# Kernel optimization log

Measured on AMD Instinct MI355X. Metric: run time of the kernel, lower is better.

Reference implementation:

```python
import jax, jax.numpy as jnp
import numpy as np

D_MODEL = 1024
N_HEADS = 16
D_HEAD = D_MODEL // N_HEADS


def setup_inputs() -> dict:
    key = jax.random.key(0)
    ks = jax.random.split(key, 9)
    s = 1.0 / np.sqrt(D_MODEL)
    def lin(kw, kb):
        W = jax.random.uniform(kw, (D_MODEL, D_MODEL), jnp.float32, -s, s)
        b = jax.random.uniform(kb, (D_MODEL,), jnp.float32, -s, s)
        return W, b
    Wq, bq = lin(ks[0], ks[1])
    Wk, bk = lin(ks[2], ks[3])
    Wv, bv = lin(ks[4], ks[5])
    Wo, bo = lin(ks[6], ks[7])
    x = jax.random.normal(ks[8], (4, 2048, D_MODEL), jnp.float32)
    return {"x": x, "Wq": Wq, "bq": bq, "Wk": Wk, "bk": bk,
            "Wv": Wv, "bv": bv, "Wo": Wo, "bo": bo}


def reference(x, Wq, bq, Wk, bk, Wv, bv, Wo, bo):
    B, T, C = x.shape
    # torch Linear: y = x @ W.T + b
    Q = x @ Wq.T + bq
    K = x @ Wk.T + bk
    V = x @ Wv.T + bv
    # [B, H, T, Dh]
    Q = Q.reshape(B, T, N_HEADS, D_HEAD).transpose(0, 2, 1, 3)
    K = K.reshape(B, T, N_HEADS, D_HEAD).transpose(0, 2, 1, 3)
    V = V.reshape(B, T, N_HEADS, D_HEAD).transpose(0, 2, 1, 3)
    scale = jnp.float32(np.sqrt(D_HEAD))
    scores = jnp.einsum('bhqd,bhkd->bhqk', Q, K) / scale
    causal = jnp.tril(jnp.ones((T, T), dtype=bool))  # True where allowed
    scores = jnp.where(causal, scores, jnp.float32(-jnp.inf))
    attn = jax.nn.softmax(scores, axis=-1)
    out = jnp.einsum('bhqk,bhkd->bhqd', attn, V)
    out = out.transpose(0, 2, 1, 3).reshape(B, T, C)
    return out @ Wo.T + bo
```

## Files before the change

### kernel.cpp

```cpp
#include <hip/hip_runtime.h>
#include <hip/hip_bf16.h>


typedef float f32x4 __attribute__((ext_vector_type(4)));
typedef __bf16 bf16x8 __attribute__((ext_vector_type(8)));

#define DEVI __device__ __forceinline__

#define QSCALE 0.1803368801111204f

template<int N> struct IC { static constexpr int value = N; };

DEVI ushort f2b(float x) {
  __hip_bfloat16 h = __float2bfloat16(x);
  return __builtin_bit_cast(ushort, h);
}

DEVI unsigned int pkbf(float a, float b) {
#if __has_builtin(__builtin_amdgcn_cvt_pk_bf16_f32)
  typedef __bf16 bf16x2 __attribute__((ext_vector_type(2)));
  bf16x2 r = __builtin_amdgcn_cvt_pk_bf16_f32(a, b);
  return __builtin_bit_cast(unsigned int, r);
#else
  return (unsigned int)f2b(a) | ((unsigned int)f2b(b) << 16);
#endif
}

DEVI bf16x8 ldsFrag(const ushort* p) {
  return __builtin_bit_cast(bf16x8, *(const uint4*)p);
}

DEVI f32x4 mfma16(bf16x8 a, bf16x8 b, f32x4 c) {
  return __builtin_amdgcn_mfma_f32_16x16x32_bf16(a, b, c, 0, 0, 0);
}

DEVI void gload_lds16(const ushort* g, ushort* l) {
  __builtin_amdgcn_global_load_lds(
      (const __attribute__((address_space(1))) unsigned int*)g,
      (__attribute__((address_space(3))) unsigned int*)l, 16, 0, 0);
}

#define SBAR() do { __builtin_amdgcn_sched_barrier(0); \
                    __builtin_amdgcn_s_barrier();      \
                    __builtin_amdgcn_sched_barrier(0); } while (0)

__global__ void k_cvtAll(const float4* __restrict__ x,
                         const float4* __restrict__ w0, const float4* __restrict__ w1,
                         const float4* __restrict__ w2, const float4* __restrict__ w3,
                         ushort4* __restrict__ xb, ushort4* __restrict__ wcat) {
  const int blk = blockIdx.x;
  const int i = blk * 256 + threadIdx.x;
  float4 f;
  ushort4* dst;
  int di;
  if (blk < 8192) {
    f = x[i]; dst = xb; di = i;
  } else {
    const int wi = i - 8192 * 256;
    const int sel = wi >> 18;
    const float4* src = (sel == 0) ? w0 : (sel == 1) ? w1 : (sel == 2) ? w2 : w3;
    f = src[wi & 262143]; dst = wcat; di = wi;
  }
  ushort4 o;
  o.x = f2b(f.x); o.y = f2b(f.y); o.z = f2b(f.z); o.w = f2b(f.w);
  dst[di] = o;
}

template<int MODE>
__global__ __launch_bounds__(512, 2)
void k_gemm(const ushort* __restrict__ A, const ushort* __restrict__ W,
            const float* __restrict__ b0, const float* __restrict__ b1,
            const float* __restrict__ b2, float* __restrict__ outF,
            ushort* __restrict__ oQ, ushort* __restrict__ oK, ushort* __restrict__ oV) {
  __shared__ ushort As[3 * 128 * 64];
  __shared__ ushort Bs[3 * 256 * 64];
  const int tid = threadIdx.x;
  const int wave = tid >> 6, lane = tid & 63;
  const int col = lane & 15, quad = lane >> 4;
  const int id = blockIdx.x;
  const int s_ = id >> 3;
  const int m0 = ((id & 7) * 8 + (s_ & 7)) * 128;
  const int n0 = (s_ >> 3) * 256;
  const int wm = (wave >> 2) * 64, wn = (wave & 3) * 64;
  f32x4 acc[4][4] = {};

  const int grow = lane >> 3;
  const int gchunk = ((lane & 7) ^ grow) * 8;
  const int cswz = col & 7;
  const ushort* Ag = A + (size_t)(m0 + wave * 16 + grow) * 1024 + gchunk;
  const ushort* Wg = W + (size_t)(n0 + wave * 32 + grow) * 1024 + gchunk;
  ushort* AsW = &As[wave * 1024];
  ushort* BsW = &Bs[wave * 2048];

  const int matId = (MODE == 0) ? (n0 >> 10) : 0;

  auto stageA = [&](int ks, int sb) {
    gload_lds16(Ag + ks,        AsW + sb * 8192);
    gload_lds16(Ag + ks + 8192, AsW + sb * 8192 + 512);
  };
  auto stageBh = [&](int ks, int sb, int h) {
    const ushort* sp = Wg + ks + h * 16384;
    ushort* dp = BsW + sb * 16384 + h * 1024;
    gload_lds16(sp,        dp);
    gload_lds16(sp + 8192, dp + 512);
  };

  auto kloop = [&](auto swc) {
    auto phase = [&](int cur, int kk, auto stagef) {
      const int ko = ((kk * 4 + quad) ^ cswz) * 8;
      const ushort* Ab = &As[cur * 8192];
      const ushort* Bb = &Bs[cur * 16384];
      bf16x8 af[4], bfr[4];
#pragma unroll
      for (int i = 0; i < 4; ++i)
        af[i] = ldsFrag(&Ab[(wm + i * 16 + col) * 64 + ko]);
#pragma unroll
      for (int j = 0; j < 4; ++j)
        bfr[j] = ldsFrag(&Bb[(wn + j * 16 + col) * 64 + ko]);
      stagef();
      SBAR();
      __builtin_amdgcn_s_setprio(1);
#pragma unroll
      for (int i = 0; i < 4; ++i)
#pragma unroll
        for (int j = 0; j < 4; ++j) {
          if constexpr (decltype(swc)::value != 0)
            acc[i][j] = mfma16(bfr[j], af[i], acc[i][j]);
          else
            acc[i][j] = mfma16(af[i], bfr[j], acc[i][j]);
        }
      __builtin_amdgcn_s_setprio(0);
    };

    stageA(0, 0);  stageBh(0, 0, 0);  stageBh(0, 0, 1);
    stageA(64, 1); stageBh(64, 1, 0); stageBh(64, 1, 1);
    asm volatile("s_waitcnt vmcnt(6)" ::: "memory");
    SBAR();

    int r0 = 0, r1 = 1, r2 = 2;
    for (int t = 0; t < 14; ++t) {
      const int ks = (t + 2) * 64;
      phase(r0, 0, [&] { stageA(ks, r2); stageBh(ks, r2, 0); });
      SBAR();
      phase(r0, 1, [&] { stageBh(ks, r2, 1); });
      asm volatile("s_waitcnt vmcnt(6)" ::: "memory");
      SBAR();
      const int tmp = r0; r0 = r1; r1 = r2; r2 = tmp;
    }
    phase(r0, 0, [&] {});
    SBAR();
    phase(r0, 1, [&] {});
    asm volatile("s_waitcnt vmcnt(0)" ::: "memory");
    SBAR();
    phase(r1, 0, [&] {});
    SBAR();
    phase(r1, 1, [&] {});
  };

  if (MODE == 1 || matId < 2) kloop(IC<1>{}); else kloop(IC<0>{});

  if (MODE == 1) {
#pragma unroll
    for (int j = 0; j < 4; ++j) {
      const int nb = n0 + wn + j * 16 + quad * 4;
      const float4 bb = *(const float4*)&b0[nb];
#pragma unroll
      for (int i = 0; i < 4; ++i) {
        const int m = m0 + wm + i * 16 + col;
        float4 v;
        v.x = acc[i][j][0] + bb.x;
        v.y = acc[i][j][1] + bb.y;
        v.z = acc[i][j][2] + bb.z;
        v.w = acc[i][j][3] + bb.w;
        *(float4*)&outF[(size_t)m * 1024 + nb] = v;
      }
    }
  } else if (matId < 2) {
    ushort* dst = (matId == 0) ? oQ : oK;
    const float* bias = (matId == 0) ? b0 : b1;
    const float sc = (matId == 0) ? QSCALE : 1.0f;
#pragma unroll
    for (int j = 0; j < 4; ++j) {
      const int nl = ((n0 & 1023) + wn + j * 16 + quad * 4);
      const int h = nl >> 6, dh0 = nl & 63;
      const float4 bb = *(const float4*)&bias[nl];
#pragma unroll
      for (int i = 0; i < 4; ++i) {
        const int m = m0 + wm + i * 16 + col;
        const int b = m >> 11, t = m & 2047;
        ushort4 pk;
        pk.x = f2b((acc[i][j][0] + bb.x) * sc);
        pk.y = f2b((acc[i][j][1] + bb.y) * sc);
        pk.z = f2b((acc[i][j][2] + bb.z) * sc);
        pk.w = f2b((acc[i][j][3] + bb.w) * sc);
        *(ushort4*)&dst[(((size_t)(b * 16 + h) * 2048) + t) * 64 + dh0] = pk;
      }
    }
  } else {
#pragma unroll
    for (int j = 0; j < 4; ++j) {
      const int nl = ((n0 & 1023) + wn + j * 16 + col);
      const int h = nl >> 6, dh = nl & 63;
      const float bn = b2[nl];
#pragma unroll
      for (int i = 0; i < 4; ++i) {
        const int mBase = m0 + wm + i * 16 + quad * 4;
        const int b = mBase >> 11, t = mBase & 2047;
        ushort4 pk;
        pk.x = f2b(acc[i][j][0] + bn);
        pk.y = f2b(acc[i][j][1] + bn);
        pk.z = f2b(acc[i][j][2] + bn);
        pk.w = f2b(acc[i][j][3] + bn);
        *(ushort4*)&oV[(((size_t)(b * 16 + h) * 64) + dh) * 2048 + t] = pk;
      }
    }
  }
}

__global__ __launch_bounds__(512, 4)
void k_attn(const ushort* __restrict__ Q, const ushort* __restrict__ K,
            const ushort* __restrict__ Vt, ushort* __restrict__ AO) {
  __shared__ ushort Ks[2 * 4096];
  __shared__ ushort Vs[2 * 4096];
  __shared__ ushort Os[512];
  __shared__ ushort Ps[16 * 16 * 72];
  const int tid = threadIdx.x;
  const int wave = tid >> 6, lane = tid & 63;
  const int col = lane & 15, quad = lane >> 4;
  const int id = blockIdx.x;
  const int bh = (id & 7) * 8 + ((id >> 3) & 7);
  const int g = id >> 6;
  const int t = (id < 256) ? (7 - g) : (g - 4);
  const int q0 = t * 256;
  const ushort* Qg = Q + (size_t)bh * 2048 * 64;
  const ushort* Kg = K + (size_t)bh * 2048 * 64;
  const ushort* Vg = Vt + (size_t)bh * 64 * 2048;

  if (tid < 128) {
    const ushort one = 0x3F80;
    ushort4 zv;
    if (tid < 8) { zv.x = one; zv.y = one; zv.z = one; zv.w = one; }
    else         { zv.x = 0;   zv.y = 0;   zv.z = 0;   zv.w = 0;   }
    *(ushort4*)&Os[tid * 4] = zv;
  }

  const int grow = lane >> 3;
  const int gchunk = ((lane & 7) ^ grow) * 8;
  const int cswz = col & 7;
  ushort* Pw0 = &Ps[((wave * 2 + 0) * 16 + col) * 72];
  ushort* Pw1 = &Ps[((wave * 2 + 1) * 16 + col) * 72];

  bf16x8 qf[2][2];
#pragma unroll
  for (int s = 0; s < 2; ++s) {
    const ushort* p = Qg + (q0 + wave * 32 + s * 16 + col) * 64 + quad * 8;
    qf[s][0] = __builtin_bit_cast(bf16x8, *(const uint4*)p);
    qf[s][1] = __builtin_bit_cast(bf16x8, *(const uint4*)(p + 32));
  }

  f32x4 o[2][4] = {};
  f32x4 la[2] = {};

  const ushort* kPtr = Kg + (wave * 8 + grow) * 64 + gchunk;
  const ushort* vPtr = Vg + (size_t)(wave * 8 + grow) * 2048 + gchunk;

  auto stage = [&](auto bufc) {
    constexpr int BUF = decltype(bufc)::value;
    gload_lds16(kPtr, &Ks[BUF * 4096 + wave * 512]);
    gload_lds16(vPtr, &Vs[BUF * 4096 + wave * 512]);
    kPtr += 64 * 64;
    vPtr += 64;
  };

  auto step = [&](auto bufc, auto maskc, int j0) {
    constexpr int BUF = decltype(bufc)::value;
    constexpr bool MASKED = (decltype(maskc)::value != 0);
    const ushort* Kb = &Ks[BUF * 4096];
    const ushort* Vb = &Vs[BUF * 4096];
    bf16x8 kf[4][2];
#pragma unroll
    for (int i = 0; i < 4; ++i) {
      kf[i][0] = ldsFrag(&Kb[(i * 16 + col) * 64 + (((0 * 4 + quad) ^ cswz) * 8)]);
      kf[i][1] = ldsFrag(&Kb[(i * 16 + col) * 64 + (((1 * 4 + quad) ^ cswz) * 8)]);
    }
#pragma unroll
    for (int s = 0; s < 2; ++s) {
      ushort* Pw = s ? Pw1 : Pw0;
      const int dlim = MASKED ? (q0 + wave * 32 + s * 16 + col - j0 - quad * 4) : 0;
#pragma unroll
      for (int i = 0; i < 4; ++i) {
        f32x4 z = {0.f, 0.f, 0.f, 0.f};
        f32x4 sv = mfma16(kf[i][0], qf[s][0], z);
        sv = mfma16(kf[i][1], qf[s][1], sv);
        if (MASKED) {
#pragma unroll
          for (int r = 0; r < 4; ++r)
            if (i * 16 + r > dlim) sv[r] = -1e30f;
        }
        f32x4 pv;
#pragma unroll
        for (int r = 0; r < 4; ++r) pv[r] = __builtin_amdgcn_exp2f(sv[r]);
        uint2 pk;
        pk.x = pkbf(pv[0], pv[1]);
        pk.y = pkbf(pv[2], pv[3]);
        *(uint2*)&Pw[i * 16 + quad * 4] = pk;
      }
    }
    bf16x8 osf = ldsFrag(&Os[col * 32 + quad * 8]);
#pragma unroll
    for (int c = 0; c < 2; ++c) {
      bf16x8 pb0 = ldsFrag(&Pw0[c * 32 + quad * 8]);
      bf16x8 pb1 = ldsFrag(&Pw1[c * 32 + quad * 8]);
      la[0] = mfma16(osf, pb0, la[0]);
      la[1] = mfma16(osf, pb1, la[1]);
#pragma unroll
      for (int i = 0; i < 4; ++i) {
        bf16x8 vf = ldsFrag(&Vb[(i * 16 + col) * 64 + (((c * 4 + quad) ^ cswz) * 8)]);
        o[0][i] = mfma16(vf, pb0, o[0][i]);
        o[1][i] = mfma16(vf, pb1, o[1][i]);
      }
    }
  };

  __syncthreads();
  stage(IC<0>{});
  for (int it2 = 0; it2 < 2 * t; ++it2) {
    __syncthreads();
    stage(IC<1>{});
    step(IC<0>{}, IC<0>{}, 0);
    __syncthreads();
    stage(IC<0>{});
    step(IC<1>{}, IC<0>{}, 0);
  }
  __syncthreads();
  stage(IC<1>{});
  step(IC<0>{}, IC<1>{}, q0);
  __syncthreads();
  stage(IC<0>{});
  if (wave >= 2) step(IC<1>{}, IC<1>{}, q0 + 64);
  __syncthreads();
  stage(IC<1>{});
  if (wave >= 4) step(IC<0>{}, IC<1>{}, q0 + 128);
  __syncthreads();
  if (wave >= 6) step(IC<1>{}, IC<1>{}, q0 + 192);

  const float invs[2] = {1.0f / __shfl(la[0][0], col), 1.0f / __shfl(la[1][0], col)};
  const int b = bh >> 4, h = bh & 15;
#pragma unroll
  for (int s = 0; s < 2; ++s) {
    const float inv = invs[s];
    const int tq = q0 + wave * 32 + s * 16 + col;
    ushort* dst = AO + (size_t)(b * 2048 + tq) * 1024 + h * 64;
#pragma unroll
    for (int i = 0; i < 4; ++i) {
      f32x4 v = o[s][i];
      ushort4 pk;
      pk.x = f2b(v[0] * inv);
      pk.y = f2b(v[1] * inv);
      pk.z = f2b(v[2] * inv);
      pk.w = f2b(v[3] * inv);
      *(ushort4*)&dst[i * 16 + quad * 4] = pk;
    }
  }
}

extern "C" void kernel_launch(void* const* d_in, const int* in_sizes, int n_in,
                              void* d_out, int out_size, void* d_ws, size_t ws_size,
                              hipStream_t stream) {
  const float* x  = (const float*)d_in[0];
  const float* Wq = (const float*)d_in[1];
  const float* bq = (const float*)d_in[2];
  const float* Wk = (const float*)d_in[3];
  const float* bk = (const float*)d_in[4];
  const float* Wv = (const float*)d_in[5];
  const float* bv = (const float*)d_in[6];
  const float* Wo = (const float*)d_in[7];
  const float* bo = (const float*)d_in[8];
  float* out = (float*)d_out;

  char* ws = (char*)d_ws;
  ushort* xb    = (ushort*)ws;
  ushort* Wcat  = (ushort*)(ws + (size_t)16 * 1024 * 1024);
  ushort* Wob   = Wcat + (size_t)3 * 1024 * 1024;
  ushort* Qh    = (ushort*)(ws + (size_t)24 * 1024 * 1024);
  ushort* Kh    = Qh + (size_t)8192 * 1024;
  ushort* Vt    = Kh + (size_t)8192 * 1024;
  ushort* AO    = Vt + (size_t)8192 * 1024;

  k_cvtAll<<<12288, 256, 0, stream>>>((const float4*)x,
                                      (const float4*)Wq, (const float4*)Wk,
                                      (const float4*)Wv, (const float4*)Wo,
                                      (ushort4*)xb, (ushort4*)Wcat);

  k_gemm<0><<<768, 512, 0, stream>>>(xb, Wcat, bq, bk, bv, nullptr, Qh, Kh, Vt);

  k_attn<<<512, 512, 0, stream>>>(Qh, Kh, Vt, AO);

  k_gemm<1><<<256, 512, 0, stream>>>(AO, Wob, bo, nullptr, nullptr, out,
                                     nullptr, nullptr, nullptr);
}
```

Measured before the change: 244.9 us.

## Use 256x256 tiles with double-buffered pipeline for QKV projection GEMM

```diff
diff --git a/kernel.cpp b/kernel.cpp
--- a/kernel.cpp
+++ b/kernel.cpp
@@ -66,12 +66,161 @@
   dst[di] = o;
 }
 
-template<int MODE>
 __global__ __launch_bounds__(512, 2)
-void k_gemm(const ushort* __restrict__ A, const ushort* __restrict__ W,
-            const float* __restrict__ b0, const float* __restrict__ b1,
-            const float* __restrict__ b2, float* __restrict__ outF,
-            ushort* __restrict__ oQ, ushort* __restrict__ oK, ushort* __restrict__ oV) {
+void k_gemm256(const ushort* __restrict__ A, const ushort* __restrict__ W,
+               const float* __restrict__ b0, const float* __restrict__ b1,
+               const float* __restrict__ b2,
+               ushort* __restrict__ oQ, ushort* __restrict__ oK,
+               ushort* __restrict__ oV) {
+  __shared__ ushort As[2][256 * 64];
+  __shared__ ushort Bs[2][256 * 64];
+  const int tid = threadIdx.x;
+  const int wave = tid >> 6, lane = tid & 63;
+  const int col = lane & 15, quad = lane >> 4;
+  const int id = blockIdx.x;
+  const int L = (id & 7) * 48 + (id >> 3);
+  const int m0 = (L & 31) * 256;
+  const int n0 = (L >> 5) * 256;
+  const int wm = (wave >> 2) * 128, wn = (wave & 3) * 64;
+  const int matId = n0 >> 10;
+
+  const int grow = lane >> 3;
+  const int gchunk = ((lane & 7) ^ grow) * 8;
+  const int cswz = col & 7;
+  const ushort* Ag = A + (size_t)(m0 + wave * 32 + grow) * 1024 + gchunk;
+  const ushort* Wg = W + (size_t)(n0 + wave * 32 + grow) * 1024 + gchunk;
+
+  f32x4 acc[8][4] = {};
+  bf16x8 bfr[4];
+
+  auto stageHalf = [&](int t1, int hf) {
+    const int buf = t1 & 1;
+    const int ks = t1 * 64;
+#pragma unroll
+    for (int u = 2 * hf; u < 2 * hf + 2; ++u) {
+      gload_lds16(Ag + (size_t)u * 8 * 1024 + ks, &As[buf][(wave * 32 + u * 8) * 64]);
+      gload_lds16(Wg + (size_t)u * 8 * 1024 + ks, &Bs[buf][(wave * 32 + u * 8) * 64]);
+    }
+  };
+
+  auto kloop = [&](auto swc) {
+    constexpr bool SW = (decltype(swc)::value != 0);
+    auto phase = [&](int p, int h, int kk, bool rdB, auto stg) {
+      const int ko = ((kk * 4 + quad) ^ cswz) * 8;
+      bf16x8 af[4];
+#pragma unroll
+      for (int i = 0; i < 4; ++i)
+        af[i] = ldsFrag(&As[p][(wm + h * 64 + i * 16 + col) * 64 + ko]);
+      if (rdB) {
+#pragma unroll
+        for (int j = 0; j < 4; ++j)
+          bfr[j] = ldsFrag(&Bs[p][(wn + j * 16 + col) * 64 + ko]);
+      }
+      stg();
+      SBAR();
+      asm volatile("s_waitcnt lgkmcnt(0)" ::: "memory");
+      __builtin_amdgcn_sched_barrier(0);
+      __builtin_amdgcn_s_setprio(1);
+#pragma unroll
+      for (int i = 0; i < 4; ++i)
+#pragma unroll
+        for (int j = 0; j < 4; ++j) {
+          if constexpr (SW)
+            acc[h * 4 + i][j] = mfma16(bfr[j], af[i], acc[h * 4 + i][j]);
+          else
+            acc[h * 4 + i][j] = mfma16(af[i], bfr[j], acc[h * 4 + i][j]);
+        }
+      __builtin_amdgcn_s_setprio(0);
+      SBAR();
+    };
+
+    stageHalf(0, 0); stageHalf(0, 1);
+    asm volatile("s_waitcnt vmcnt(0)" ::: "memory");
+    SBAR();
+
+    for (int t = 0; t < 16; ++t) {
+      const int p = t & 1;
+      const bool st = (t < 15);
+      phase(p, 0, 0, true,  [&] { if (st) stageHalf(t + 1, 0); });
+      phase(p, 1, 0, false, [&] { if (st) stageHalf(t + 1, 1); });
+      phase(p, 0, 1, true,  [&] {});
+      {
+        const int ko = ((1 * 4 + quad) ^ cswz) * 8;
+        bf16x8 af[4];
+#pragma unroll
+        for (int i = 0; i < 4; ++i)
+          af[i] = ldsFrag(&As[p][(wm + 64 + i * 16 + col) * 64 + ko]);
+        SBAR();
+        asm volatile("s_waitcnt lgkmcnt(0)" ::: "memory");
+        __builtin_amdgcn_sched_barrier(0);
+        __builtin_amdgcn_s_setprio(1);
+#pragma unroll
+        for (int i = 0; i < 4; ++i)
+#pragma unroll
+          for (int j = 0; j < 4; ++j) {
+            if constexpr (SW)
+              acc[4 + i][j] = mfma16(bfr[j], af[i], acc[4 + i][j]);
+            else
+              acc[4 + i][j] = mfma16(af[i], bfr[j], acc[4 + i][j]);
+          }
+        __builtin_amdgcn_s_setprio(0);
+        if (st) { asm volatile("s_waitcnt vmcnt(0)" ::: "memory"); }
+        SBAR();
+      }
+    }
+  };
+
+  if (matId < 2) kloop(IC<1>{}); else kloop(IC<0>{});
+
+  if (matId < 2) {
+    ushort* dst = (matId == 0) ? oQ : oK;
+    const float* bias = (matId == 0) ? b0 : b1;
+    const float sc = (matId == 0) ? QSCALE : 1.0f;
+#pragma unroll
+    for (int h = 0; h < 2; ++h)
+#pragma unroll
+      for (int j = 0; j < 4; ++j) {
+        const int nl = (n0 & 1023) + wn + j * 16 + quad * 4;
+        const int hh = nl >> 6, dh0 = nl & 63;
+        const float4 bb = *(const float4*)&bias[nl];
+#pragma unroll
+        for (int i = 0; i < 4; ++i) {
+          const int m = m0 + wm + h * 64 + i * 16 + col;
+          const int b = m >> 11, t = m & 2047;
+          ushort4 pk;
+          pk.x = f2b((acc[h * 4 + i][j][0] + bb.x) * sc);
+          pk.y = f2b((acc[h * 4 + i][j][1] + bb.y) * sc);
+          pk.z = f2b((acc[h * 4 + i][j][2] + bb.z) * sc);
+          pk.w = f2b((acc[h * 4 + i][j][3] + bb.w) * sc);
+          *(ushort4*)&dst[(((size_t)(b * 16 + hh) * 2048) + t) * 64 + dh0] = pk;
+        }
+      }
+  } else {
+#pragma unroll
+    for (int h = 0; h < 2; ++h)
+#pragma unroll
+      for (int j = 0; j < 4; ++j) {
+        const int nl = (n0 & 1023) + wn + j * 16 + col;
+        const int hh = nl >> 6, dh = nl & 63;
+        const float bn = b2[nl];
+#pragma unroll
+        for (int i = 0; i < 4; ++i) {
+          const int mBase = m0 + wm + h * 64 + i * 16 + quad * 4;
+          const int b = mBase >> 11, t = mBase & 2047;
+          ushort4 pk;
+          pk.x = f2b(acc[h * 4 + i][j][0] + bn);
+          pk.y = f2b(acc[h * 4 + i][j][1] + bn);
+          pk.z = f2b(acc[h * 4 + i][j][2] + bn);
+          pk.w = f2b(acc[h * 4 + i][j][3] + bn);
+          *(ushort4*)&oV[(((size_t)(b * 16 + hh) * 64) + dh) * 2048 + t] = pk;
+        }
+      }
+  }
+}
+
+__global__ __launch_bounds__(512, 2)
+void k_gemmP(const ushort* __restrict__ A, const ushort* __restrict__ W,
+             const float* __restrict__ b0, float* __restrict__ outF) {
   __shared__ ushort As[3 * 128 * 64];
   __shared__ ushort Bs[3 * 256 * 64];
   const int tid = threadIdx.x;
@@ -92,8 +241,6 @@
   ushort* AsW = &As[wave * 1024];
   ushort* BsW = &Bs[wave * 2048];
 
-  const int matId = (MODE == 0) ? (n0 >> 10) : 0;
-
   auto stageA = [&](int ks, int sb) {
     gload_lds16(Ag + ks,        AsW + sb * 8192);
     gload_lds16(Ag + ks + 8192, AsW + sb * 8192 + 512);
@@ -105,114 +252,65 @@
     gload_lds16(sp + 8192, dp + 512);
   };
 
-  auto kloop = [&](auto swc) {
-    auto phase = [&](int cur, int kk, auto stagef) {
-      const int ko = ((kk * 4 + quad) ^ cswz) * 8;
-      const ushort* Ab = &As[cur * 8192];
-      const ushort* Bb = &Bs[cur * 16384];
-      bf16x8 af[4], bfr[4];
-#pragma unroll
-      for (int i = 0; i < 4; ++i)
-        af[i] = ldsFrag(&Ab[(wm + i * 16 + col) * 64 + ko]);
+  auto phase = [&](int cur, int kk, auto stagef) {
+    const int ko = ((kk * 4 + quad) ^ cswz) * 8;
+    const ushort* Ab = &As[cur * 8192];
+    const ushort* Bb = &Bs[cur * 16384];
+    bf16x8 af[4], bfr[4];
+#pragma unroll
+    for (int i = 0; i < 4; ++i)
+      af[i] = ldsFrag(&Ab[(wm + i * 16 + col) * 64 + ko]);
+#pragma unroll
+    for (int j = 0; j < 4; ++j)
+      bfr[j] = ldsFrag(&Bb[(wn + j * 16 + col) * 64 + ko]);
+    stagef();
+    SBAR();
+    __builtin_amdgcn_s_setprio(1);
+#pragma unroll
+    for (int i = 0; i < 4; ++i)
 #pragma unroll
       for (int j = 0; j < 4; ++j)
-        bfr[j] = ldsFrag(&Bb[(wn + j * 16 + col) * 64 + ko]);
-      stagef();
-      SBAR();
-      __builtin_amdgcn_s_setprio(1);
-#pragma unroll
-      for (int i = 0; i < 4; ++i)
-#pragma unroll
-        for (int j = 0; j < 4; ++j) {
-          if constexpr (decltype(swc)::value != 0)
-            acc[i][j] = mfma16(bfr[j], af[i], acc[i][j]);
-          else
-            acc[i][j] = mfma16(af[i], bfr[j], acc[i][j]);
-        }
-      __builtin_amdgcn_s_setprio(0);
-    };
-
-    stageA(0, 0);  stageBh(0, 0, 0);  stageBh(0, 0, 1);
-    stageA(64, 1); stageBh(64, 1, 0); stageBh(64, 1, 1);
+        acc[i][j] = mfma16(bfr[j], af[i], acc[i][j]);
+    __builtin_amdgcn_s_setprio(0);
+  };
+
+  stageA(0, 0);  stageBh(0, 0, 0);  stageBh(0, 0, 1);
+  stageA(64, 1); stageBh(64, 1, 0); stageBh(64, 1, 1);
+  asm volatile("s_waitcnt vmcnt(6)" ::: "memory");
+  SBAR();
+
+  int r0 = 0, r1 = 1, r2 = 2;
+  for (int t = 0; t < 14; ++t) {
+    const int ks = (t + 2) * 64;
+    phase(r0, 0, [&] { stageA(ks, r2); stageBh(ks, r2, 0); });
+    SBAR();
+    phase(r0, 1, [&] { stageBh(ks, r2, 1); });
     asm volatile("s_waitcnt vmcnt(6)" ::: "memory");
     SBAR();
-
-    int r0 = 0, r1 = 1, r2 = 2;
-    for (int t = 0; t < 14; ++t) {
-      const int ks = (t + 2) * 64;
-      phase(r0, 0, [&] { stageA(ks, r2); stageBh(ks, r2, 0); });
-      SBAR();
-      phase(r0, 1, [&] { stageBh(ks, r2, 1); });
-      asm volatile("s_waitcnt vmcnt(6)" ::: "memory");
-      SBAR();
-      const int tmp = r0; r0 = r1; r1 = r2; r2 = tmp;
-    }
-    phase(r0, 0, [&] {});
-    SBAR();
-    phase(r0, 1, [&] {});
-    asm volatile("s_waitcnt vmcnt(0)" ::: "memory");
-    SBAR();
-    phase(r1, 0, [&] {});
-    SBAR();
-    phase(r1, 1, [&] {});
-  };
-
-  if (MODE == 1 || matId < 2) kloop(IC<1>{}); else kloop(IC<0>{});
-
-  if (MODE == 1) {
-#pragma unroll
-    for (int j = 0; j < 4; ++j) {
-      const int nb = n0 + wn + j * 16 + quad * 4;
-      const float4 bb = *(const float4*)&b0[nb];
-#pragma unroll
-      for (int i = 0; i < 4; ++i) {
-        const int m = m0 + wm + i * 16 + col;
-        float4 v;
-        v.x = acc[i][j][0] + bb.x;
-        v.y = acc[i][j][1] + bb.y;
-        v.z = acc[i][j][2] + bb.z;
-        v.w = acc[i][j][3] + bb.w;
-        *(float4*)&outF[(size_t)m * 1024 + nb] = v;
-      }
-    }
-  } else if (matId < 2) {
-    ushort* dst = (matId == 0) ? oQ : oK;
-    const float* bias = (matId == 0) ? b0 : b1;
-    const float sc = (matId == 0) ? QSCALE : 1.0f;
-#pragma unroll
-    for (int j = 0; j < 4; ++j) {
-      const int nl = ((n0 & 1023) + wn + j * 16 + quad * 4);
-      const int h = nl >> 6, dh0 = nl & 63;
-      const float4 bb = *(const float4*)&bias[nl];
-#pragma unroll
-      for (int i = 0; i < 4; ++i) {
-        const int m = m0 + wm + i * 16 + col;
-        const int b = m >> 11, t = m & 2047;
-        ushort4 pk;
-        pk.x = f2b((acc[i][j][0] + bb.x) * sc);
-        pk.y = f2b((acc[i][j][1] + bb.y) * sc);
-        pk.z = f2b((acc[i][j][2] + bb.z) * sc);
-        pk.w = f2b((acc[i][j][3] + bb.w) * sc);
-        *(ushort4*)&dst[(((size_t)(b * 16 + h) * 2048) + t) * 64 + dh0] = pk;
-      }
-    }
-  } else {
-#pragma unroll
-    for (int j = 0; j < 4; ++j) {
-      const int nl = ((n0 & 1023) + wn + j * 16 + col);
-      const int h = nl >> 6, dh = nl & 63;
-      const float bn = b2[nl];
-#pragma unroll
-      for (int i = 0; i < 4; ++i) {
-        const int mBase = m0 + wm + i * 16 + quad * 4;
-        const int b = mBase >> 11, t = mBase & 2047;
-        ushort4 pk;
-        pk.x = f2b(acc[i][j][0] + bn);
-        pk.y = f2b(acc[i][j][1] + bn);
-        pk.z = f2b(acc[i][j][2] + bn);
-        pk.w = f2b(acc[i][j][3] + bn);
-        *(ushort4*)&oV[(((size_t)(b * 16 + h) * 64) + dh) * 2048 + t] = pk;
-      }
+    const int tmp = r0; r0 = r1; r1 = r2; r2 = tmp;
+  }
+  phase(r0, 0, [&] {});
+  SBAR();
+  phase(r0, 1, [&] {});
+  asm volatile("s_waitcnt vmcnt(0)" ::: "memory");
+  SBAR();
+  phase(r1, 0, [&] {});
+  SBAR();
+  phase(r1, 1, [&] {});
+
+#pragma unroll
+  for (int j = 0; j < 4; ++j) {
+    const int nb = n0 + wn + j * 16 + quad * 4;
+    const float4 bb = *(const float4*)&b0[nb];
+#pragma unroll
+    for (int i = 0; i < 4; ++i) {
+      const int m = m0 + wm + i * 16 + col;
+      float4 v;
+      v.x = acc[i][j][0] + bb.x;
+      v.y = acc[i][j][1] + bb.y;
+      v.z = acc[i][j][2] + bb.z;
+      v.w = acc[i][j][3] + bb.w;
+      *(float4*)&outF[(size_t)m * 1024 + nb] = v;
     }
   }
 }
@@ -392,10 +490,9 @@
                                       (const float4*)Wv, (const float4*)Wo,
                                       (ushort4*)xb, (ushort4*)Wcat);
 
-  k_gemm<0><<<768, 512, 0, stream>>>(xb, Wcat, bq, bk, bv, nullptr, Qh, Kh, Vt);
+  k_gemm256<<<384, 512, 0, stream>>>(xb, Wcat, bq, bk, bv, Qh, Kh, Vt);
 
   k_attn<<<512, 512, 0, stream>>>(Qh, Kh, Vt, AO);
 
-  k_gemm<1><<<256, 512, 0, stream>>>(AO, Wob, bo, nullptr, nullptr, out,
-                                     nullptr, nullptr, nullptr);
-}
+  k_gemmP<<<256, 512, 0, stream>>>(AO, Wob, bo, out);
+}
```

New measurement: 254.8 us. 1.04x slower.

## Add QKV GEMM kernel loading weight fragments directly to registers with smaller tiles

Applied to the files above, without the earlier changes.

```diff
diff --git a/kernel.cpp b/kernel.cpp
--- a/kernel.cpp
+++ b/kernel.cpp
@@ -66,12 +66,140 @@
   dst[di] = o;
 }
 
-template<int MODE>
+__global__ __launch_bounds__(256, 3)
+void k_gemmB(const ushort* __restrict__ A, const ushort* __restrict__ W,
+             const float* __restrict__ b0, const float* __restrict__ b1,
+             const float* __restrict__ b2,
+             ushort* __restrict__ oQ, ushort* __restrict__ oK,
+             ushort* __restrict__ oV) {
+  __shared__ ushort As[2][128 * 64];
+  const int tid = threadIdx.x;
+  const int wave = tid >> 6, lane = tid & 63;
+  const int col = lane & 15, quad = lane >> 4;
+  const int id = blockIdx.x;
+  const int m0 = ((id & 7) * 8 + ((id >> 3) & 7)) * 128;
+  const int n0 = (id >> 6) * 128;
+  const int wm = (wave >> 1) * 64, wn = (wave & 1) * 64;
+  const int matId = n0 >> 10;
+
+  const int grow = lane >> 3;
+  const int gchunk = ((lane & 7) ^ grow) * 8;
+  const int cswz = col & 7;
+  const ushort* Ag = A + (size_t)(m0 + wave * 8 + grow) * 1024 + gchunk;
+
+  const ushort* bAddr[4];
+#pragma unroll
+  for (int j = 0; j < 4; ++j)
+    bAddr[j] = W + (size_t)(n0 + wn + j * 16 + col) * 1024 + quad * 8;
+
+  f32x4 acc[4][4] = {};
+  bf16x8 bkA[4], bkB[4];
+
+  auto stageA = [&](int t1) {
+    const int p = t1 & 1;
+    const int ks = t1 * 64;
+#pragma unroll
+    for (int g = 0; g < 4; ++g)
+      gload_lds16(Ag + (size_t)g * 32 * 1024 + ks, &As[p][wave * 512 + g * 2048]);
+  };
+  auto loadB = [&](bf16x8 (&d)[4], int t1, int kk) {
+#pragma unroll
+    for (int j = 0; j < 4; ++j)
+      d[j] = __builtin_bit_cast(bf16x8, *(const uint4*)(bAddr[j] + t1 * 64 + kk * 32));
+  };
+
+  auto kloop = [&](auto swc) {
+    constexpr bool SW = (decltype(swc)::value != 0);
+    stageA(0);
+    __builtin_amdgcn_sched_barrier(0);
+    loadB(bkA, 0, 0);
+    loadB(bkB, 0, 1);
+    asm volatile("s_waitcnt vmcnt(8)" ::: "memory");
+    SBAR();
+    for (int t = 0; t < 16; ++t) {
+      const int p = t & 1;
+      stageA(t + 1);
+      __builtin_amdgcn_sched_barrier(0);
+      {
+        bf16x8 af[4];
+#pragma unroll
+        for (int i = 0; i < 4; ++i)
+          af[i] = ldsFrag(&As[p][(wm + i * 16 + col) * 64 + ((0 * 4 + quad) ^ cswz) * 8]);
+#pragma unroll
+        for (int i = 0; i < 4; ++i)
+#pragma unroll
+          for (int j = 0; j < 4; ++j) {
+            if constexpr (SW) acc[i][j] = mfma16(bkA[j], af[i], acc[i][j]);
+            else              acc[i][j] = mfma16(af[i], bkA[j], acc[i][j]);
+          }
+        loadB(bkA, t + 1, 0);
+      }
+      {
+        bf16x8 af[4];
+#pragma unroll
+        for (int i = 0; i < 4; ++i)
+          af[i] = ldsFrag(&As[p][(wm + i * 16 + col) * 64 + ((1 * 4 + quad) ^ cswz) * 8]);
+#pragma unroll
+        for (int i = 0; i < 4; ++i)
+#pragma unroll
+          for (int j = 0; j < 4; ++j) {
+            if constexpr (SW) acc[i][j] = mfma16(bkB[j], af[i], acc[i][j]);
+            else              acc[i][j] = mfma16(af[i], bkB[j], acc[i][j]);
+          }
+        loadB(bkB, t + 1, 1);
+      }
+      asm volatile("s_waitcnt vmcnt(8)" ::: "memory");
+      SBAR();
+    }
+  };
+
+  if (matId < 2) kloop(IC<1>{}); else kloop(IC<0>{});
+
+  if (matId < 2) {
+    ushort* dst = (matId == 0) ? oQ : oK;
+    const float* bias = (matId == 0) ? b0 : b1;
+    const float sc = (matId == 0) ? QSCALE : 1.0f;
+#pragma unroll
+    for (int j = 0; j < 4; ++j) {
+      const int nl = ((n0 & 1023) + wn + j * 16 + quad * 4);
+      const int h = nl >> 6, dh0 = nl & 63;
+      const float4 bb = *(const float4*)&bias[nl];
+#pragma unroll
+      for (int i = 0; i < 4; ++i) {
+        const int m = m0 + wm + i * 16 + col;
+        const int b = m >> 11, t = m & 2047;
+        ushort4 pk;
+        pk.x = f2b((acc[i][j][0] + bb.x) * sc);
+        pk.y = f2b((acc[i][j][1] + bb.y) * sc);
+        pk.z = f2b((acc[i][j][2] + bb.z) * sc);
+        pk.w = f2b((acc[i][j][3] + bb.w) * sc);
+        *(ushort4*)&dst[(((size_t)(b * 16 + h) * 2048) + t) * 64 + dh0] = pk;
+      }
+    }
+  } else {
+#pragma unroll
+    for (int j = 0; j < 4; ++j) {
+      const int nl = ((n0 & 1023) + wn + j * 16 + col);
+      const int h = nl >> 6, dh = nl & 63;
+      const float bn = b2[nl];
+#pragma unroll
+      for (int i = 0; i < 4; ++i) {
+        const int mBase = m0 + wm + i * 16 + quad * 4;
+        const int b = mBase >> 11, t = mBase & 2047;
+        ushort4 pk;
+        pk.x = f2b(acc[i][j][0] + bn);
+        pk.y = f2b(acc[i][j][1] + bn);
+        pk.z = f2b(acc[i][j][2] + bn);
+        pk.w = f2b(acc[i][j][3] + bn);
+        *(ushort4*)&oV[(((size_t)(b * 16 + h) * 64) + dh) * 2048 + t] = pk;
+      }
+    }
+  }
+}
+
 __global__ __launch_bounds__(512, 2)
-void k_gemm(const ushort* __restrict__ A, const ushort* __restrict__ W,
-            const float* __restrict__ b0, const float* __restrict__ b1,
-            const float* __restrict__ b2, float* __restrict__ outF,
-            ushort* __restrict__ oQ, ushort* __restrict__ oK, ushort* __restrict__ oV) {
+void k_gemmP(const ushort* __restrict__ A, const ushort* __restrict__ W,
+             const float* __restrict__ b0, float* __restrict__ outF) {
   __shared__ ushort As[3 * 128 * 64];
   __shared__ ushort Bs[3 * 256 * 64];
   const int tid = threadIdx.x;
@@ -92,8 +220,6 @@
   ushort* AsW = &As[wave * 1024];
   ushort* BsW = &Bs[wave * 2048];
 
-  const int matId = (MODE == 0) ? (n0 >> 10) : 0;
-
   auto stageA = [&](int ks, int sb) {
     gload_lds16(Ag + ks,        AsW + sb * 8192);
     gload_lds16(Ag + ks + 8192, AsW + sb * 8192 + 512);
@@ -105,114 +231,65 @@
     gload_lds16(sp + 8192, dp + 512);
   };
 
-  auto kloop = [&](auto swc) {
-    auto phase = [&](int cur, int kk, auto stagef) {
-      const int ko = ((kk * 4 + quad) ^ cswz) * 8;
-      const ushort* Ab = &As[cur * 8192];
-      const ushort* Bb = &Bs[cur * 16384];
-      bf16x8 af[4], bfr[4];
-#pragma unroll
-      for (int i = 0; i < 4; ++i)
-        af[i] = ldsFrag(&Ab[(wm + i * 16 + col) * 64 + ko]);
+  auto phase = [&](int cur, int kk, auto stagef) {
+    const int ko = ((kk * 4 + quad) ^ cswz) * 8;
+    const ushort* Ab = &As[cur * 8192];
+    const ushort* Bb = &Bs[cur * 16384];
+    bf16x8 af[4], bfr[4];
+#pragma unroll
+    for (int i = 0; i < 4; ++i)
+      af[i] = ldsFrag(&Ab[(wm + i * 16 + col) * 64 + ko]);
+#pragma unroll
+    for (int j = 0; j < 4; ++j)
+      bfr[j] = ldsFrag(&Bb[(wn + j * 16 + col) * 64 + ko]);
+    stagef();
+    SBAR();
+    __builtin_amdgcn_s_setprio(1);
+#pragma unroll
+    for (int i = 0; i < 4; ++i)
 #pragma unroll
       for (int j = 0; j < 4; ++j)
-        bfr[j] = ldsFrag(&Bb[(wn + j * 16 + col) * 64 + ko]);
-      stagef();
-      SBAR();
-      __builtin_amdgcn_s_setprio(1);
-#pragma unroll
-      for (int i = 0; i < 4; ++i)
-#pragma unroll
-        for (int j = 0; j < 4; ++j) {
-          if constexpr (decltype(swc)::value != 0)
-            acc[i][j] = mfma16(bfr[j], af[i], acc[i][j]);
-          else
-            acc[i][j] = mfma16(af[i], bfr[j], acc[i][j]);
-        }
-      __builtin_amdgcn_s_setprio(0);
-    };
-
-    stageA(0, 0);  stageBh(0, 0, 0);  stageBh(0, 0, 1);
-    stageA(64, 1); stageBh(64, 1, 0); stageBh(64, 1, 1);
+        acc[i][j] = mfma16(bfr[j], af[i], acc[i][j]);
+    __builtin_amdgcn_s_setprio(0);
+  };
+
+  stageA(0, 0);  stageBh(0, 0, 0);  stageBh(0, 0, 1);
+  stageA(64, 1); stageBh(64, 1, 0); stageBh(64, 1, 1);
+  asm volatile("s_waitcnt vmcnt(6)" ::: "memory");
+  SBAR();
+
+  int r0 = 0, r1 = 1, r2 = 2;
+  for (int t = 0; t < 14; ++t) {
+    const int ks = (t + 2) * 64;
+    phase(r0, 0, [&] { stageA(ks, r2); stageBh(ks, r2, 0); });
+    SBAR();
+    phase(r0, 1, [&] { stageBh(ks, r2, 1); });
     asm volatile("s_waitcnt vmcnt(6)" ::: "memory");
     SBAR();
-
-    int r0 = 0, r1 = 1, r2 = 2;
-    for (int t = 0; t < 14; ++t) {
-      const int ks = (t + 2) * 64;
-      phase(r0, 0, [&] { stageA(ks, r2); stageBh(ks, r2, 0); });
-      SBAR();
-      phase(r0, 1, [&] { stageBh(ks, r2, 1); });
-      asm volatile("s_waitcnt vmcnt(6)" ::: "memory");
-      SBAR();
-      const int tmp = r0; r0 = r1; r1 = r2; r2 = tmp;
-    }
-    phase(r0, 0, [&] {});
-    SBAR();
-    phase(r0, 1, [&] {});
-    asm volatile("s_waitcnt vmcnt(0)" ::: "memory");
-    SBAR();
-    phase(r1, 0, [&] {});
-    SBAR();
-    phase(r1, 1, [&] {});
-  };
-
-  if (MODE == 1 || matId < 2) kloop(IC<1>{}); else kloop(IC<0>{});
-
-  if (MODE == 1) {
-#pragma unroll
-    for (int j = 0; j < 4; ++j) {
-      const int nb = n0 + wn + j * 16 + quad * 4;
-      const float4 bb = *(const float4*)&b0[nb];
-#pragma unroll
-      for (int i = 0; i < 4; ++i) {
-        const int m = m0 + wm + i * 16 + col;
-        float4 v;
-        v.x = acc[i][j][0] + bb.x;
-        v.y = acc[i][j][1] + bb.y;
-        v.z = acc[i][j][2] + bb.z;
-        v.w = acc[i][j][3] + bb.w;
-        *(float4*)&outF[(size_t)m * 1024 + nb] = v;
-      }
-    }
-  } else if (matId < 2) {
-    ushort* dst = (matId == 0) ? oQ : oK;
-    const float* bias = (matId == 0) ? b0 : b1;
-    const float sc = (matId == 0) ? QSCALE : 1.0f;
-#pragma unroll
-    for (int j = 0; j < 4; ++j) {
-      const int nl = ((n0 & 1023) + wn + j * 16 + quad * 4);
-      const int h = nl >> 6, dh0 = nl & 63;
-      const float4 bb = *(const float4*)&bias[nl];
-#pragma unroll
-      for (int i = 0; i < 4; ++i) {
-        const int m = m0 + wm + i * 16 + col;
-        const int b = m >> 11, t = m & 2047;
-        ushort4 pk;
-        pk.x = f2b((acc[i][j][0] + bb.x) * sc);
-        pk.y = f2b((acc[i][j][1] + bb.y) * sc);
-        pk.z = f2b((acc[i][j][2] + bb.z) * sc);
-        pk.w = f2b((acc[i][j][3] + bb.w) * sc);
-        *(ushort4*)&dst[(((size_t)(b * 16 + h) * 2048) + t) * 64 + dh0] = pk;
-      }
-    }
-  } else {
-#pragma unroll
-    for (int j = 0; j < 4; ++j) {
-      const int nl = ((n0 & 1023) + wn + j * 16 + col);
-      const int h = nl >> 6, dh = nl & 63;
-      const float bn = b2[nl];
-#pragma unroll
-      for (int i = 0; i < 4; ++i) {
-        const int mBase = m0 + wm + i * 16 + quad * 4;
-        const int b = mBase >> 11, t = mBase & 2047;
-        ushort4 pk;
-        pk.x = f2b(acc[i][j][0] + bn);
-        pk.y = f2b(acc[i][j][1] + bn);
-        pk.z = f2b(acc[i][j][2] + bn);
-        pk.w = f2b(acc[i][j][3] + bn);
-        *(ushort4*)&oV[(((size_t)(b * 16 + h) * 64) + dh) * 2048 + t] = pk;
-      }
+    const int tmp = r0; r0 = r1; r1 = r2; r2 = tmp;
+  }
+  phase(r0, 0, [&] {});
+  SBAR();
+  phase(r0, 1, [&] {});
+  asm volatile("s_waitcnt vmcnt(0)" ::: "memory");
+  SBAR();
+  phase(r1, 0, [&] {});
+  SBAR();
+  phase(r1, 1, [&] {});
+
+#pragma unroll
+  for (int j = 0; j < 4; ++j) {
+    const int nb = n0 + wn + j * 16 + quad * 4;
+    const float4 bb = *(const float4*)&b0[nb];
+#pragma unroll
+    for (int i = 0; i < 4; ++i) {
+      const int m = m0 + wm + i * 16 + col;
+      float4 v;
+      v.x = acc[i][j][0] + bb.x;
+      v.y = acc[i][j][1] + bb.y;
+      v.z = acc[i][j][2] + bb.z;
+      v.w = acc[i][j][3] + bb.w;
+      *(float4*)&outF[(size_t)m * 1024 + nb] = v;
     }
   }
 }
@@ -392,10 +469,9 @@
                                       (const float4*)Wv, (const float4*)Wo,
                                       (ushort4*)xb, (ushort4*)Wcat);
 
-  k_gemm<0><<<768, 512, 0, stream>>>(xb, Wcat, bq, bk, bv, nullptr, Qh, Kh, Vt);
+  k_gemmB<<<1536, 256, 0, stream>>>(xb, Wcat, bq, bk, bv, Qh, Kh, Vt);
 
   k_attn<<<512, 512, 0, stream>>>(Qh, Kh, Vt, AO);
 
-  k_gemm<1><<<256, 512, 0, stream>>>(AO, Wob, bo, nullptr, nullptr, out,
-                                     nullptr, nullptr, nullptr);
-}
+  k_gemmP<<<256, 512, 0, stream>>>(AO, Wob, bo, out);
+}
```

Measured after the change: 298.1 us. 1.22x slower.
